# Kernel tuning notes

Hardware: AMD Instinct MI355X
Metric: run time of the kernel (lower is better)

## Reference

```python
import jax, jax.numpy as jnp
import numpy as np

N = 50000      # nodes
E = 800000     # edges
D = 128        # in_dim == out_dim
H = 8          # heads
DH = D // H    # head dim = 16
BN_EPS = 1e-5


def batch_norm(x, gamma, beta):
    # BatchNorm1d in training mode: biased variance over the node/batch axis.
    mu = jnp.mean(x, axis=0)
    var = jnp.mean((x - mu) ** 2, axis=0)
    return (x - mu) * jax.lax.rsqrt(var + BN_EPS) * gamma + beta


def setup_inputs() -> dict:
    key = jax.random.key(0)
    ks = jax.random.split(key, 16)
    inp = {
        'src': jax.random.randint(ks[0], (E,), 0, N),
        'dst': jax.random.randint(ks[1], (E,), 0, N),
        'h': jax.random.normal(ks[2], (N, D), jnp.float32),
        'e': jax.random.normal(ks[3], (E, D), jnp.float32),
        'h_in': jax.random.normal(ks[4], (N, D), jnp.float32),  # unused: overwritten by h in forward
        # attention projections (bias=False)
        'Wq': jax.random.normal(ks[5], (D, D), jnp.float32) / np.sqrt(D),
        'Wk': jax.random.normal(ks[6], (D, D), jnp.float32) / np.sqrt(D),
        'Wv': jax.random.normal(ks[7], (D, D), jnp.float32) / np.sqrt(D),
        'We': jax.random.normal(ks[8], (D, D), jnp.float32) / np.sqrt(D),
        # sdp_layer (bias=True)
        'W_sdp': jax.random.normal(ks[9], (D, D), jnp.float32) / np.sqrt(D),
        'b_sdp': jnp.zeros((D,), jnp.float32),
        # FFN out_h / out_h_2
        'W_h1': jax.random.normal(ks[10], (D, 2 * D), jnp.float32) / np.sqrt(D),
        'b_h1': jnp.zeros((2 * D,), jnp.float32),
        'W_h2': jax.random.normal(ks[11], (2 * D, D), jnp.float32) / np.sqrt(2 * D),
        'b_h2': jnp.zeros((D,), jnp.float32),
        # batch_norm_1 (shared across both BN applications)
        'bn_gamma': jnp.ones((D,), jnp.float32),
        'bn_beta': jnp.zeros((D,), jnp.float32),
    }
    return inp


def reference(src, dst, h, e, h_in, Wq, Wk, Wv, We, W_sdp, b_sdp,
              W_h1, b_h1, W_h2, b_h2, bn_gamma, bn_beta):
    h_res = h  # h_in = h inside forward

    # --- MultiHeadAttention (default path: all edges real, sum aggregation) ---
    q = (h @ Wq).reshape(N, H, DH)
    k = (h @ Wk).reshape(N, H, DH)
    v = (h @ Wv).reshape(N, H, DH)   # v = v_linear(h_in) with h_in == h
    ef = (e @ We).reshape(E, H, DH)

    # src_dot_dst -> scaling -> imp_exp_attn: elementwise K_src*Q_dst / sqrt(dh) * E
    score = (k[src] * q[dst]) / np.sqrt(DH) * ef          # [E, H, DH]
    # exp('score'): exp(clamp(sum_d score, -5, 5)), keepdim
    score_soft = jnp.exp(jnp.clip(score.sum(-1), -5.0, 5.0))[..., None]  # [E, H, 1]

    aV = jax.ops.segment_sum(v[src] * score_soft, dst, num_segments=N)   # [N, H, DH]
    z = jax.ops.segment_sum(score_soft, dst, num_segments=N)             # [N, H, 1]
    h_attn = (aV / (z + 1e-6)).reshape(N, D)

    # --- EncoderLayer post-attention (dropout=0 -> identity) ---
    hx = h_attn @ W_sdp + b_sdp
    hx = h_res + hx
    hx = batch_norm(hx, bn_gamma, bn_beta)

    h_in2 = hx
    ff = jax.nn.relu(hx @ W_h1 + b_h1) @ W_h2 + b_h2
    hx = h_in2 + ff
    hx = batch_norm(hx, bn_gamma, bn_beta)

    # edge_learning=False: e returned unchanged
    return hx, e
```

## Files before the change

### kernel.cpp

```cpp
#include <hip/hip_runtime.h>
#include <hip/hip_bf16.h>
#include <math.h>

#define N_NODES 50000
#define E_EDGES 800000
#define D_DIM   128
#define H_HEADS 8

typedef __attribute__((ext_vector_type(8))) short short8;
typedef __attribute__((ext_vector_type(4))) float f32x4;
typedef unsigned int   uint_t;
typedef unsigned short ushort_t;

static __device__ __forceinline__ float4 ldg4(const float* p) {
    return *reinterpret_cast<const float4*>(p);
}
static __device__ __forceinline__ ushort_t f2bf(float x) {
    union { float f; uint_t u; } v; v.f = x;
    uint_t r = v.u + 0x7fffu + ((v.u >> 16) & 1u);
    return (ushort_t)(r >> 16);
}
static __device__ __forceinline__ float bf2f(ushort_t b) {
    union { uint_t u; float f; } v; v.u = ((uint_t)b) << 16;
    return v.f;
}
static __device__ __forceinline__ uint_t pk(float lo, float hi) {
    return (uint_t)f2bf(lo) | ((uint_t)f2bf(hi) << 16);
}

__global__ void hist_kernel(const int* __restrict__ dst, int* __restrict__ hist) {
    int i = blockIdx.x * blockDim.x + threadIdx.x;
    if (i < E_EDGES) atomicAdd(&hist[dst[i]], 1);
}

__global__ __launch_bounds__(1024) void scan_kernel(const int* __restrict__ cnt,
                                                    int* __restrict__ start,
                                                    int* __restrict__ cursor) {
    __shared__ int sh[1024];
    const int t = threadIdx.x;
    const int CPT = (N_NODES + 1023) / 1024;
    int lo = t * CPT;
    int hi = lo + CPT; if (hi > N_NODES) hi = N_NODES; if (lo > N_NODES) lo = N_NODES;
    int s = 0;
    for (int i = lo; i < hi; i++) s += cnt[i];
    sh[t] = s;
    __syncthreads();
    for (int off = 1; off < 1024; off <<= 1) {
        int v = (t >= off) ? sh[t - off] : 0;
        __syncthreads();
        sh[t] += v;
        __syncthreads();
    }
    int run = sh[t] - s;
    for (int i = lo; i < hi; i++) {
        start[i]  = run;
        cursor[i] = run;
        run += cnt[i];
    }
    if (t == 1023) start[N_NODES] = sh[1023];
}

__global__ void scatter_kernel(const int* __restrict__ src, const int* __restrict__ dst,
                               int* __restrict__ cursor,
                               int* __restrict__ rank, int* __restrict__ srcs) {
    int i = blockIdx.x * blockDim.x + threadIdx.x;
    if (i < E_EDGES) {
        int p = atomicAdd(&cursor[dst[i]], 1);
        rank[i] = p;
        srcs[p] = src[i];
    }
}

__global__ __launch_bounds__(256) void prep_weights(const float* __restrict__ Wq,
                                                    const float* __restrict__ Wk,
                                                    const float* __restrict__ Wv,
                                                    const float* __restrict__ We,
                                                    const float* __restrict__ Wsdp,
                                                    const float* __restrict__ Wh1,
                                                    const float* __restrict__ Wh2,
                                                    ushort_t* __restrict__ prep) {
    const int b = blockIdx.x;
    const float* W; int ld, cb, kc;
    if (b < 6)       { W = (b < 2 ? Wq : (b < 4 ? Wk : Wv)); ld = 128; cb = 0; kc = b & 1; }
    else if (b < 8)  { W = We;   ld = 128; cb = 0;            kc = b - 6; }
    else if (b < 10) { W = Wsdp; ld = 128; cb = 0;            kc = b - 8; }
    else if (b < 14) { W = Wh1;  ld = 256; cb = (b - 10) >> 1; kc = (b - 10) & 1; }
    else             { W = Wh2;  ld = 128; cb = 0;            kc = b - 14; }
    char* tile = (char*)(prep + (size_t)b * 8192);
    for (int i = threadIdx.x; i < 8192; i += 256) {
        int col = i >> 6, kl = i & 63;
        int k = kc * 64 + kl;
        float v = W[(size_t)k * ld + cb * 128 + col];
        int byte = (col * 128 + kl * 2) ^ ((col & 7) << 4);
        *(ushort_t*)(tile + byte) = f2bf(v);
    }
}

__global__ __launch_bounds__(256) void prep_we_frag(const float* __restrict__ We,
                                                    ushort_t* __restrict__ WeF) {
    int slot = blockIdx.x * 256 + threadIdx.x;
    if (slot < 2048) {
        int lane = slot & 63;
        int kc   = (slot >> 6) & 3;
        int cg   = slot >> 8;
        int col  = cg * 16 + (lane & 15);
        int kb   = kc * 32 + ((lane >> 4) << 3);
#pragma unroll
        for (int j = 0; j < 8; j++)
            WeF[slot * 8 + j] = f2bf(We[(size_t)(kb + j) * 128 + col]);
    }
}

template<int ROWS, int OBF, int ABF, int RESMODE, int SADD, int ASS>
__global__ __launch_bounds__(256) void gemm_bf16(const void* __restrict__ Av,
                                                 int M, int K,
                                                 const ushort_t* __restrict__ Bt, int nkc,
                                                 const float* __restrict__ bias,
                                                 const void* __restrict__ residv,
                                                 void* __restrict__ Cv, int ldc,
                                                 size_t cbStride, int doRelu,
                                                 float* __restrict__ sums,
                                                 const float* __restrict__ ss) {
    constexpr int MI  = ROWS / 32;
    constexpr int TPR = 256 / ROWS;
    constexpr int KPT = 64 / TPR;
    __shared__ __align__(16) unsigned char As[ROWS * 128];
    __shared__ __align__(16) unsigned char Bs[16384];
    __shared__ float csum[128], csq[128];
    const int tid  = threadIdx.x;
    const int lane = tid & 63;
    const int wid  = tid >> 6;
    const int wr   = wid >> 1;
    const int wc   = wid & 1;
    const int cb   = blockIdx.y;
    const int row0 = blockIdx.x * ROWS;

    if (SADD && tid < 128) { csum[tid] = 0.f; csq[tid] = 0.f; }

    f32x4 acc[MI][4];
#pragma unroll
    for (int i = 0; i < MI; i++)
#pragma unroll
        for (int j = 0; j < 4; j++) acc[i][j] = (f32x4){0.f, 0.f, 0.f, 0.f};

    for (int kc = 0; kc < nkc; kc++) {
        __syncthreads();
        {
            int row = tid / TPR;
            int kl0 = (tid % TPR) * KPT;
            int gr  = row0 + row;
            int s = (row & 7) << 4;
            if (ABF) {
                const ushort_t* A16 = (const ushort_t*)Av;
#pragma unroll
                for (int j = 0; j < KPT / 8; j++) {
                    uint4 w = make_uint4(0, 0, 0, 0);
                    if (gr < M) w = *(const uint4*)(&A16[(size_t)gr * K + kc * 64 + kl0 + 8 * j]);
                    int byte = (row * 128 + (kl0 + 8 * j) * 2) ^ s;
                    *(uint4*)(As + byte) = w;
                }
            } else {
                const float* A = (const float*)Av;
                float4 v4[KPT / 4];
                if (gr < M) {
                    const float* ap = &A[(size_t)gr * K + kc * 64 + kl0];
#pragma unroll
                    for (int j = 0; j < KPT / 4; j++) v4[j] = ldg4(ap + 4 * j);
                } else {
#pragma unroll
                    for (int j = 0; j < KPT / 4; j++) v4[j] = make_float4(0.f, 0.f, 0.f, 0.f);
                }
                if (ASS) {
#pragma unroll
                    for (int j = 0; j < KPT / 4; j++) {
                        int kk = kc * 64 + kl0 + 4 * j;
                        v4[j].x = v4[j].x * ss[kk + 0] + ss[128 + kk + 0];
                        v4[j].y = v4[j].y * ss[kk + 1] + ss[128 + kk + 1];
                        v4[j].z = v4[j].z * ss[kk + 2] + ss[128 + kk + 2];
                        v4[j].w = v4[j].w * ss[kk + 3] + ss[128 + kk + 3];
                    }
                }
#pragma unroll
                for (int j = 0; j < KPT / 8; j++) {
                    uint4 w;
                    w.x = pk(v4[2 * j].x, v4[2 * j].y);
                    w.y = pk(v4[2 * j].z, v4[2 * j].w);
                    w.z = pk(v4[2 * j + 1].x, v4[2 * j + 1].y);
                    w.w = pk(v4[2 * j + 1].z, v4[2 * j + 1].w);
                    int byte = (row * 128 + (kl0 + 8 * j) * 2) ^ s;
                    *(uint4*)(As + byte) = w;
                }
            }
        }
        {
            const uint4* gB = (const uint4*)(Bt + (size_t)(cb * nkc + kc) * 8192);
#pragma unroll
            for (int j = 0; j < 4; j++) {
                int idx = j * 256 + tid;
                ((uint4*)Bs)[idx] = gB[idx];
            }
        }
        __syncthreads();
#pragma unroll
        for (int k0 = 0; k0 < 64; k0 += 32) {
            short8 a[MI], b[4];
#pragma unroll
            for (int mi = 0; mi < MI; mi++) {
                int row = wr * (ROWS / 2) + mi * 16 + (lane & 15);
                int byte = (row * 128 + k0 * 2 + (lane >> 4) * 16) ^ ((row & 7) << 4);
                a[mi] = *(const short8*)(As + byte);
            }
#pragma unroll
            for (int ni = 0; ni < 4; ni++) {
                int col = wc * 64 + ni * 16 + (lane & 15);
                int byte = (col * 128 + k0 * 2 + (lane >> 4) * 16) ^ ((col & 7) << 4);
                b[ni] = *(const short8*)(Bs + byte);
            }
#pragma unroll
            for (int mi = 0; mi < MI; mi++)
#pragma unroll
                for (int ni = 0; ni < 4; ni++)
                    acc[mi][ni] = __builtin_amdgcn_mfma_f32_16x16x32_bf16(a[mi], b[ni], acc[mi][ni], 0, 0, 0);
        }
    }

    float colS[4] = {0.f, 0.f, 0.f, 0.f};
    float colQ[4] = {0.f, 0.f, 0.f, 0.f};
#pragma unroll
    for (int mi = 0; mi < MI; mi++) {
#pragma unroll
        for (int r = 0; r < 4; r++) {
            int row = row0 + wr * (ROWS / 2) + mi * 16 + ((lane >> 4) << 2) + r;
            if (row < M) {
#pragma unroll
                for (int ni = 0; ni < 4; ni++) {
                    int col = wc * 64 + ni * 16 + (lane & 15);
                    float v = acc[mi][ni][r];
                    if (bias) v += bias[cb * 128 + col];
                    if (doRelu) v = fmaxf(v, 0.f);
                    if (residv) {
                        if (RESMODE == 1) {
                            v += bf2f(((const ushort_t*)residv)[(size_t)row * ldc + col]);
                        } else if (RESMODE == 2) {
                            float rr = ((const float*)residv)[(size_t)row * ldc + col];
                            v += rr * ss[col] + ss[128 + col];
                        } else {
                            v += ((const float*)residv)[(size_t)row * ldc + col];
                        }
                    }
                    if (SADD) { colS[ni] += v; colQ[ni] += v * v; }
                    if (OBF) ((ushort_t*)Cv)[cb * cbStride + (size_t)row * ldc + col] = f2bf(v);
                    else     ((float*)Cv)[cb * cbStride + (size_t)row * ldc + col] = v;
                }
            }
        }
    }
    if (SADD) {
#pragma unroll
        for (int ni = 0; ni < 4; ni++) {
            int col = wc * 64 + ni * 16 + (lane & 15);
            atomicAdd(&csum[col], colS[ni]);
            atomicAdd(&csq[col],  colQ[ni]);
        }
        __syncthreads();
        if (tid < 128) {
            atomicAdd(&sums[tid],       csum[tid]);
            atomicAdd(&sums[128 + tid], csq[tid]);
        }
    }
}

__global__ __launch_bounds__(256, 6) void edge_mfma(const float* __restrict__ e,
                                                    const int* __restrict__ src,
                                                    const int* __restrict__ dst,
                                                    const ushort_t* __restrict__ Qm,
                                                    const ushort_t* __restrict__ Km,
                                                    const ushort_t* __restrict__ WeF,
                                                    const int* __restrict__ rank,
                                                    ushort_t* __restrict__ S16,
                                                    float* __restrict__ out_e) {
    __shared__ __align__(16) unsigned char Asm[16384];
    const int tid  = threadIdx.x;
    const int lane = tid & 63;
    const int wid  = tid >> 6;
    const int e0   = blockIdx.x * 64;

#pragma unroll
    for (int it = 0; it < 2; it++) {
        int row = (tid >> 3) + it * 32;
        int c0  = (tid & 7) * 16;
        const float* ep = &e[(size_t)(e0 + row) * 128 + c0];
        float*       op = &out_e[(size_t)(e0 + row) * 128 + c0];
        float4 v4[4];
#pragma unroll
        for (int j = 0; j < 4; j++) v4[j] = ldg4(ep + 4 * j);
#pragma unroll
        for (int j = 0; j < 4; j++) *(float4*)(op + 4 * j) = v4[j];
        int chunk = c0 >> 6;
        int klb   = (c0 & 63) * 2;
        int s     = (row & 7) << 4;
        uint4 w0, w1;
        w0.x = pk(v4[0].x, v4[0].y); w0.y = pk(v4[0].z, v4[0].w);
        w0.z = pk(v4[1].x, v4[1].y); w0.w = pk(v4[1].z, v4[1].w);
        w1.x = pk(v4[2].x, v4[2].y); w1.y = pk(v4[2].z, v4[2].w);
        w1.z = pk(v4[3].x, v4[3].y); w1.w = pk(v4[3].z, v4[3].w);
        *(uint4*)(Asm + chunk * 8192 + ((row * 128 + klb) ^ s))      = w0;
        *(uint4*)(Asm + chunk * 8192 + ((row * 128 + klb + 16) ^ s)) = w1;
    }
    __syncthreads();

    f32x4 acc[8];
#pragma unroll
    for (int i = 0; i < 8; i++) acc[i] = (f32x4){0.f, 0.f, 0.f, 0.f};

#pragma unroll
    for (int k0 = 0; k0 < 128; k0 += 32) {
        int chunk = k0 >> 6;
        int klb   = (k0 & 63) * 2;
        int kc    = k0 >> 5;
        short8 a;
        {
            int arow = wid * 16 + (lane & 15);
            int byte = chunk * 8192 + ((arow * 128 + klb + (lane >> 4) * 16) ^ ((arow & 7) << 4));
            a = *(const short8*)(Asm + byte);
        }
#pragma unroll
        for (int ni = 0; ni < 8; ni++) {
            short8 b = *(const short8*)(WeF + ((size_t)((ni * 4 + kc) * 64 + lane)) * 8);
            acc[ni] = __builtin_amdgcn_mfma_f32_16x16x32_bf16(a, b, acc[ni], 0, 0, 0);
        }
    }

    const int rows0 = e0 + wid * 16 + ((lane >> 4) << 2);
    int sidx[4], didx[4];
#pragma unroll
    for (int r = 0; r < 4; r++) {
        sidx[r] = src[rows0 + r];
        didx[r] = dst[rows0 + r];
    }
    const int myr = lane & 15;
    float sc[8];
#pragma unroll
    for (int ni = 0; ni < 8; ni++) {
        int col = ni * 16 + (lane & 15);
        float pv[4];
#pragma unroll
        for (int r = 0; r < 4; r++) {
            float kv = bf2f(Km[(size_t)sidx[r] * 128 + col]);
            float qv = bf2f(Qm[(size_t)didx[r] * 128 + col]);
            pv[r] = acc[ni][r] * kv * qv;
        }
#pragma unroll
        for (int off = 1; off < 16; off <<= 1)
#pragma unroll
            for (int r = 0; r < 4; r++) pv[r] += __shfl_xor(pv[r], off, 64);
        float mv = (myr == 0) ? pv[0] : (myr == 1) ? pv[1] : (myr == 2) ? pv[2] : pv[3];
        sc[ni] = __expf(fminf(fmaxf(0.25f * mv, -5.f), 5.f));
    }
    if (myr < 4) {
        int rk = rank[rows0 + myr];
        uint4 u;
        u.x = pk(sc[0], sc[1]); u.y = pk(sc[2], sc[3]);
        u.z = pk(sc[4], sc[5]); u.w = pk(sc[6], sc[7]);
        *(uint4*)&S16[(size_t)rk * 8] = u;
    }
}

__global__ __launch_bounds__(256) void agg_kernel(const uint_t* __restrict__ Vu,
                                                  const ushort_t* __restrict__ S16,
                                                  const int* __restrict__ start,
                                                  const int* __restrict__ srcs,
                                                  uint_t* __restrict__ HAu) {
    const int lane = threadIdx.x & 63;
    const int n = blockIdx.x * 4 + (threadIdx.x >> 6);
    if (n >= N_NODES) return;
    const int s0 = start[n];
    const int s1 = start[n + 1];
    const int h  = lane >> 3;
    float a0 = 0.f, a1 = 0.f, z = 0.f;
    int i = s0;
    for (; i + 4 <= s1; i += 4) {
        int m0 = srcs[i], m1 = srcs[i + 1], m2 = srcs[i + 2], m3 = srcs[i + 3];
        float t0 = bf2f(S16[(size_t)i * 8 + h]);
        float t1 = bf2f(S16[(size_t)(i + 1) * 8 + h]);
        float t2 = bf2f(S16[(size_t)(i + 2) * 8 + h]);
        float t3 = bf2f(S16[(size_t)(i + 3) * 8 + h]);
        uint_t v0 = Vu[(size_t)m0 * 64 + lane];
        uint_t v1 = Vu[(size_t)m1 * 64 + lane];
        uint_t v2 = Vu[(size_t)m2 * 64 + lane];
        uint_t v3 = Vu[(size_t)m3 * 64 + lane];
        a0 = fmaf(t0, bf2f((ushort_t)v0), a0); a1 = fmaf(t0, bf2f((ushort_t)(v0 >> 16)), a1);
        a0 = fmaf(t1, bf2f((ushort_t)v1), a0); a1 = fmaf(t1, bf2f((ushort_t)(v1 >> 16)), a1);
        a0 = fmaf(t2, bf2f((ushort_t)v2), a0); a1 = fmaf(t2, bf2f((ushort_t)(v2 >> 16)), a1);
        a0 = fmaf(t3, bf2f((ushort_t)v3), a0); a1 = fmaf(t3, bf2f((ushort_t)(v3 >> 16)), a1);
        z += t0 + t1 + t2 + t3;
    }
    for (; i < s1; i++) {
        int m = srcs[i];
        float t = bf2f(S16[(size_t)i * 8 + h]);
        uint_t v = Vu[(size_t)m * 64 + lane];
        a0 = fmaf(t, bf2f((ushort_t)v), a0);
        a1 = fmaf(t, bf2f((ushort_t)(v >> 16)), a1);
        z += t;
    }
    float inv = 1.f / (z + 1e-6f);
    HAu[(size_t)n * 64 + lane] = pk(a0 * inv, a1 * inv);
}

__global__ void bn_finalize(const float* __restrict__ sums,
                            const float* __restrict__ gamma,
                            const float* __restrict__ beta,
                            float* __restrict__ ss) {
    int c = threadIdx.x;
    float mu  = sums[c] * (1.f / (float)N_NODES);
    float var = sums[128 + c] * (1.f / (float)N_NODES) - mu * mu;
    float scale = rsqrtf(var + 1e-5f) * gamma[c];
    ss[c]       = scale;
    ss[128 + c] = beta[c] - mu * scale;
}

__global__ __launch_bounds__(256) void bn_apply_f32(const float* __restrict__ X,
                                                    const float* __restrict__ ss,
                                                    float* __restrict__ Y) {
    const size_t total = (size_t)N_NODES * 128;
    const size_t step = (size_t)gridDim.x * blockDim.x * 4;
    for (size_t i = ((size_t)blockIdx.x * blockDim.x + threadIdx.x) * 4; i < total; i += step) {
        float4 x = ldg4(&X[i]);
        int c = (int)(i & 127);
        float4 y;
        y.x = x.x * ss[c + 0] + ss[128 + c + 0];
        y.y = x.y * ss[c + 1] + ss[128 + c + 1];
        y.z = x.z * ss[c + 2] + ss[128 + c + 2];
        y.w = x.w * ss[c + 3] + ss[128 + c + 3];
        *(float4*)(&Y[i]) = y;
    }
}

extern "C" void kernel_launch(void* const* d_in, const int* in_sizes, int n_in,
                              void* d_out, int out_size, void* d_ws, size_t ws_size,
                              hipStream_t stream) {
    (void)in_sizes; (void)n_in; (void)out_size; (void)ws_size;
    const int*   src   = (const int*)d_in[0];
    const int*   dst   = (const int*)d_in[1];
    const float* h     = (const float*)d_in[2];
    const float* e     = (const float*)d_in[3];
    const float* Wq    = (const float*)d_in[5];
    const float* Wk    = (const float*)d_in[6];
    const float* Wv    = (const float*)d_in[7];
    const float* We    = (const float*)d_in[8];
    const float* Wsdp  = (const float*)d_in[9];
    const float* bsdp  = (const float*)d_in[10];
    const float* Wh1   = (const float*)d_in[11];
    const float* bh1   = (const float*)d_in[12];
    const float* Wh2   = (const float*)d_in[13];
    const float* bh2   = (const float*)d_in[14];
    const float* gamma = (const float*)d_in[15];
    const float* beta  = (const float*)d_in[16];
    float* out = (float*)d_out;

    float* ws = (float*)d_ws;
    const size_t NM = (size_t)N_NODES * 128;
    ushort_t* Q16  = (ushort_t*)ws;
    ushort_t* K16  = Q16 + NM;
    ushort_t* V16  = Q16 + 2 * NM;
    ushort_t* HA16 = (ushort_t*)(ws + 3 * NM / 2);
    float*    Kb   = ws + 2 * NM;
    ushort_t* S16  = (ushort_t*)(ws + 3 * NM);
    float*    T1r  = ws + 4 * NM;
    ushort_t* T16  = (ushort_t*)T1r;
    float*    STATS = ws + 6 * NM;
    int* hist   = (int*)(STATS + 1024);
    int* startp = hist + N_NODES;
    int* cursor = startp + N_NODES + 1;
    ushort_t* prep = (ushort_t*)(((uintptr_t)(cursor + N_NODES) + 255) & ~(uintptr_t)255);
    ushort_t* WeF  = prep + (size_t)18 * 8192;

    int* rank = (int*)T1r;
    int* srcs = rank + E_EDGES;

    float* sums1 = STATS;
    float* ss1   = STATS + 256;
    float* sums2 = STATS + 512;
    float* ss2   = STATS + 768;

    prep_weights<<<18, 256, 0, stream>>>(Wq, Wk, Wv, We, Wsdp, Wh1, Wh2, prep);
    prep_we_frag<<<8, 256, 0, stream>>>(We, WeF);

    hipMemsetAsync(STATS, 0, (1024 + N_NODES) * sizeof(float), stream);

    hist_kernel<<<(E_EDGES + 255) / 256, 256, 0, stream>>>(dst, hist);
    scan_kernel<<<1, 1024, 0, stream>>>(hist, startp, cursor);
    scatter_kernel<<<(E_EDGES + 255) / 256, 256, 0, stream>>>(src, dst, cursor, rank, srcs);

    const int rt128 = (N_NODES + 127) / 128;
    const int rt64  = (N_NODES + 63) / 64;

    gemm_bf16<128, 1, 0, 0, 0, 0><<<dim3(rt128, 3), 256, 0, stream>>>(
        h, N_NODES, 128, prep, 2, nullptr, nullptr, Q16, 128, NM, 0, nullptr, nullptr);

    edge_mfma<<<E_EDGES / 64, 256, 0, stream>>>(e, src, dst, Q16, K16, WeF,
                                                rank, S16, out + NM);

    agg_kernel<<<(N_NODES + 3) / 4, 256, 0, stream>>>((const uint_t*)V16, S16, startp, srcs,
                                                      (uint_t*)HA16);

    gemm_bf16<64, 0, 1, 0, 1, 0><<<dim3(rt64, 1), 256, 0, stream>>>(
        HA16, N_NODES, 128, prep + (size_t)8 * 8192, 2, bsdp, h, Kb, 128, 0, 0, sums1, nullptr);

    bn_finalize<<<1, 128, 0, stream>>>(sums1, gamma, beta, ss1);

    gemm_bf16<128, 1, 0, 0, 0, 1><<<dim3(rt128, 2), 256, 0, stream>>>(
        Kb, N_NODES, 128, prep + (size_t)10 * 8192, 2, bh1, nullptr, T16, 256, 128, 1, nullptr, ss1);
    gemm_bf16<64, 0, 1, 2, 1, 0><<<dim3(rt64, 1), 256, 0, stream>>>(
        T16, N_NODES, 256, prep + (size_t)14 * 8192, 4, bh2, Kb, Kb, 128, 0, 0, sums2, ss1);

    bn_finalize<<<1, 128, 0, stream>>>(sums2, gamma, beta, ss2);
    bn_apply_f32<<<2048, 256, 0, stream>>>(Kb, ss2, out);
}
```

Measured before the change: 787.3 us.

## Restructure edge_mfma into 8-wave 2x4 tiling with early K/Q gathers

The edge score kernel now runs 512 threads per 64-edge block with waves laid out 2 (rows) by 4 (head groups). Each wave computes a 32x32 output tile. The random K/Q gathers and src/dst/rank index loads are issued before the shared-memory staging and MFMA loop, so their latency overlaps the e tile load and matrix work. Per-edge head scores go through a small LDS buffer so one coalesced 16-byte store is made per edge. This adds an extra barrier, a different occupancy profile and more registers held live across the MFMA loop.

```diff
diff --git a/kernel.cpp b/kernel.cpp
--- a/kernel.cpp
+++ b/kernel.cpp
@@ -270,7 +270,7 @@
     }
 }
 
-__global__ __launch_bounds__(256, 6) void edge_mfma(const float* __restrict__ e,
+__global__ __launch_bounds__(512, 8) void edge_mfma(const float* __restrict__ e,
                                                     const int* __restrict__ src,
                                                     const int* __restrict__ dst,
                                                     const ushort_t* __restrict__ Qm,
@@ -280,20 +280,49 @@
                                                     ushort_t* __restrict__ S16,
                                                     float* __restrict__ out_e) {
     __shared__ __align__(16) unsigned char Asm[16384];
+    __shared__ __align__(16) ushort_t sm[64][8];
     const int tid  = threadIdx.x;
     const int lane = tid & 63;
     const int wid  = tid >> 6;
+    const int wr   = wid >> 2;
+    const int wc   = wid & 3;
     const int e0   = blockIdx.x * 64;
 
-#pragma unroll
-    for (int it = 0; it < 2; it++) {
-        int row = (tid >> 3) + it * 32;
-        int c0  = (tid & 7) * 16;
-        const float* ep = &e[(size_t)(e0 + row) * 128 + c0];
-        float*       op = &out_e[(size_t)(e0 + row) * 128 + c0];
-        float4 v4[4];
-#pragma unroll
-        for (int j = 0; j < 4; j++) v4[j] = ldg4(ep + 4 * j);
+    int rk = (tid < 64) ? rank[e0 + tid] : 0;
+    int sidx[2][4], didx[2][4];
+#pragma unroll
+    for (int mi = 0; mi < 2; mi++) {
+        int rb = e0 + wr * 32 + mi * 16 + ((lane >> 4) << 2);
+#pragma unroll
+        for (int r = 0; r < 4; r++) {
+            sidx[mi][r] = src[rb + r];
+            didx[mi][r] = dst[rb + r];
+        }
+    }
+
+    const int row = tid >> 3;
+    const int c0  = (tid & 7) * 16;
+    const float* ep = &e[(size_t)(e0 + row) * 128 + c0];
+    float4 v4[4];
+#pragma unroll
+    for (int j = 0; j < 4; j++) v4[j] = ldg4(ep + 4 * j);
+
+    float kq[2][2][4];
+#pragma unroll
+    for (int mi = 0; mi < 2; mi++)
+#pragma unroll
+        for (int ni = 0; ni < 2; ni++) {
+            const int col = (wc * 2 + ni) * 16 + (lane & 15);
+#pragma unroll
+            for (int r = 0; r < 4; r++) {
+                float kv = bf2f(Km[(size_t)sidx[mi][r] * 128 + col]);
+                float qv = bf2f(Qm[(size_t)didx[mi][r] * 128 + col]);
+                kq[mi][ni][r] = kv * qv * 0.25f;
+            }
+        }
+
+    {
+        float* op = &out_e[(size_t)(e0 + row) * 128 + c0];
 #pragma unroll
         for (int j = 0; j < 4; j++) *(float4*)(op + 4 * j) = v4[j];
         int chunk = c0 >> 6;
@@ -309,59 +338,59 @@
     }
     __syncthreads();
 
-    f32x4 acc[8];
-#pragma unroll
-    for (int i = 0; i < 8; i++) acc[i] = (f32x4){0.f, 0.f, 0.f, 0.f};
+    f32x4 acc[2][2];
+#pragma unroll
+    for (int i = 0; i < 2; i++)
+#pragma unroll
+        for (int j = 0; j < 2; j++) acc[i][j] = (f32x4){0.f, 0.f, 0.f, 0.f};
 
 #pragma unroll
     for (int k0 = 0; k0 < 128; k0 += 32) {
         int chunk = k0 >> 6;
         int klb   = (k0 & 63) * 2;
         int kc    = k0 >> 5;
-        short8 a;
-        {
-            int arow = wid * 16 + (lane & 15);
+        short8 a[2];
+#pragma unroll
+        for (int mi = 0; mi < 2; mi++) {
+            int arow = wr * 32 + mi * 16 + (lane & 15);
             int byte = chunk * 8192 + ((arow * 128 + klb + (lane >> 4) * 16) ^ ((arow & 7) << 4));
-            a = *(const short8*)(Asm + byte);
-        }
-#pragma unroll
-        for (int ni = 0; ni < 8; ni++) {
-            short8 b = *(const short8*)(WeF + ((size_t)((ni * 4 + kc) * 64 + lane)) * 8);
-            acc[ni] = __builtin_amdgcn_mfma_f32_16x16x32_bf16(a, b, acc[ni], 0, 0, 0);
-        }
-    }
-
-    const int rows0 = e0 + wid * 16 + ((lane >> 4) << 2);
-    int sidx[4], didx[4];
-#pragma unroll
-    for (int r = 0; r < 4; r++) {
-        sidx[r] = src[rows0 + r];
-        didx[r] = dst[rows0 + r];
-    }
-    const int myr = lane & 15;
-    float sc[8];
-#pragma unroll
-    for (int ni = 0; ni < 8; ni++) {
-        int col = ni * 16 + (lane & 15);
-        float pv[4];
-#pragma unroll
-        for (int r = 0; r < 4; r++) {
-            float kv = bf2f(Km[(size_t)sidx[r] * 128 + col]);
-            float qv = bf2f(Qm[(size_t)didx[r] * 128 + col]);
-            pv[r] = acc[ni][r] * kv * qv;
-        }
-#pragma unroll
-        for (int off = 1; off < 16; off <<= 1)
-#pragma unroll
-            for (int r = 0; r < 4; r++) pv[r] += __shfl_xor(pv[r], off, 64);
-        float mv = (myr == 0) ? pv[0] : (myr == 1) ? pv[1] : (myr == 2) ? pv[2] : pv[3];
-        sc[ni] = __expf(fminf(fmaxf(0.25f * mv, -5.f), 5.f));
-    }
-    if (myr < 4) {
-        int rk = rank[rows0 + myr];
-        uint4 u;
-        u.x = pk(sc[0], sc[1]); u.y = pk(sc[2], sc[3]);
-        u.z = pk(sc[4], sc[5]); u.w = pk(sc[6], sc[7]);
+            a[mi] = *(const short8*)(Asm + byte);
+        }
+#pragma unroll
+        for (int ni = 0; ni < 2; ni++) {
+            int cg = wc * 2 + ni;
+            short8 b = *(const short8*)(WeF + ((size_t)((cg * 4 + kc) * 64 + lane)) * 8);
+#pragma unroll
+            for (int mi = 0; mi < 2; mi++)
+                acc[mi][ni] = __builtin_amdgcn_mfma_f32_16x16x32_bf16(a[mi], b, acc[mi][ni], 0, 0, 0);
+        }
+    }
+
+#pragma unroll
+    for (int mi = 0; mi < 2; mi++) {
+        const int er0 = wr * 32 + mi * 16 + ((lane >> 4) << 2);
+#pragma unroll
+        for (int ni = 0; ni < 2; ni++) {
+            const int head = wc * 2 + ni;
+            float pv[4];
+#pragma unroll
+            for (int r = 0; r < 4; r++) pv[r] = acc[mi][ni][r] * kq[mi][ni][r];
+#pragma unroll
+            for (int off = 1; off < 16; off <<= 1)
+#pragma unroll
+                for (int r = 0; r < 4; r++) pv[r] += __shfl_xor(pv[r], off, 64);
+            if ((lane & 15) == 0) {
+#pragma unroll
+                for (int r = 0; r < 4; r++) {
+                    float v = fminf(fmaxf(pv[r], -5.f), 5.f);
+                    sm[er0 + r][head] = f2bf(__expf(v));
+                }
+            }
+        }
+    }
+    __syncthreads();
+    if (tid < 64) {
+        uint4 u = *(const uint4*)&sm[tid][0];
         *(uint4*)&S16[(size_t)rk * 8] = u;
     }
 }
@@ -498,7 +527,7 @@
     gemm_bf16<128, 1, 0, 0, 0, 0><<<dim3(rt128, 3), 256, 0, stream>>>(
         h, N_NODES, 128, prep, 2, nullptr, nullptr, Q16, 128, NM, 0, nullptr, nullptr);
 
-    edge_mfma<<<E_EDGES / 64, 256, 0, stream>>>(e, src, dst, Q16, K16, WeF,
+    edge_mfma<<<E_EDGES / 64, 512, 0, stream>>>(e, src, dst, Q16, K16, WeF,
                                                 rank, S16, out + NM);
 
     agg_kernel<<<(N_NODES + 3) / 4, 256, 0, stream>>>((const uint_t*)V16, S16, startp, srcs,
```

New measurement: 813.6 us. 1.03x slower.
